# Kernel optimization log

Measured on AMD Instinct MI355X. Metric: run time of the kernel, lower is better.

Reference implementation:

```python
import jax, jax.numpy as jnp
import numpy as np

RATE_NUM = 8
MAX_RATE = 256
C = 256


def setup_inputs() -> dict:
    key = jax.random.key(0)
    k1, k2, k3, k4 = jax.random.split(key, 4)
    B, H, W = 4, 32, 32
    x = jax.random.normal(k1, (B, MAX_RATE, H, W), dtype=jnp.float32)
    indexes = jax.random.randint(k2, (B * H * W,), 0, RATE_NUM, dtype=jnp.int64)
    # kaiming_normal_(a=sqrt(5)) on (rate_num, max_rate, C): fan_in = C (last dim),
    # gain = sqrt(2/(1+a^2)) = sqrt(1/3), std = gain/sqrt(fan_in)
    std = np.sqrt(1.0 / 3.0) / np.sqrt(C)
    weight = jax.random.normal(k3, (RATE_NUM, MAX_RATE, C), dtype=jnp.float32) * std
    bound = 1.0 / np.sqrt(RATE_NUM)
    bias = jax.random.uniform(k4, (RATE_NUM, C), dtype=jnp.float32, minval=-bound, maxval=bound)
    return {"x": x, "indexes": indexes, "weight": weight, "bias": bias}


def reference(x, indexes, weight, bias):
    B, R, H, W = x.shape  # R == max_rate
    L = H * W
    x_blr = x.reshape(B, R, L).transpose(0, 2, 1)          # (B, L, R)
    w = weight[indexes].reshape(B, L, R, -1)               # (B, L, R, C)
    b = bias[indexes].reshape(B, L, -1)                    # (B, L, C)
    out = jnp.einsum('blr,blrc->blc', x_blr, w) + b        # per-token GEMV
    return out.reshape(B, H, W, -1).transpose(0, 3, 1, 2)  # (B, C, H, W)
```

## Files before the change

### kernel.cpp

```cpp
#include <hip/hip_runtime.h>


#define C_DIM 256
#define KD    256

typedef __attribute__((ext_vector_type(8))) short bf16x8;
typedef __attribute__((ext_vector_type(4))) float f32x4;

__device__ inline short f2bf(float f) {
    union { float f; unsigned u; } v; v.f = f;
    return (short)((v.u + 0x7FFFu + ((v.u >> 16) & 1u)) >> 16);
}

__global__ __launch_bounds__(256) void fused_mfma_kernel(
    const float* __restrict__ x,
    const int*   __restrict__ idx,
    const float* __restrict__ weight,
    const float* __restrict__ bias,
    float*       __restrict__ out)
{
    const int t    = threadIdx.x;
    const int lane = t & 63;
    const int wav  = t >> 6;
    const int quad = lane >> 4;
    const int li   = lane & 15;

    const int j   = blockIdx.z;
    const int c0  = blockIdx.x * 128 + (wav & 1) * 64;
    const int lg0 = blockIdx.y * 128 + (wav >> 1) * 64;
    const int b   = lg0 >> 10;
    const int l0  = lg0 & 1023;

    const float* __restrict__ wp = weight + j * (KD * C_DIM) + (quad * 8) * C_DIM + c0 + li;
    const float* __restrict__ xp = x + (b << 18) + ((quad * 8) << 10) + l0 + li;

    f32x4 acc[4][4];
    #pragma unroll
    for (int mt = 0; mt < 4; ++mt)
        #pragma unroll
        for (int nt = 0; nt < 4; ++nt)
            acc[mt][nt] = (f32x4){0.f, 0.f, 0.f, 0.f};

    for (int kc = 0; kc < KD; kc += 32) {
        bf16x8 af[4], bfr[4];
        #pragma unroll
        for (int mt = 0; mt < 4; ++mt) {
            const float* __restrict__ p = wp + kc * C_DIM + mt * 16;
            #pragma unroll
            for (int i = 0; i < 8; ++i) af[mt][i] = f2bf(p[i * C_DIM]);
        }
        #pragma unroll
        for (int nt = 0; nt < 4; ++nt) {
            const float* __restrict__ p = xp + (kc << 10) + nt * 16;
            #pragma unroll
            for (int i = 0; i < 8; ++i) bfr[nt][i] = f2bf(p[i << 10]);
        }
        #pragma unroll
        for (int mt = 0; mt < 4; ++mt)
            #pragma unroll
            for (int nt = 0; nt < 4; ++nt)
                acc[mt][nt] = __builtin_amdgcn_mfma_f32_16x16x32_bf16(
                    af[mt], bfr[nt], acc[mt][nt], 0, 0, 0);
    }

    #pragma unroll
    for (int mt = 0; mt < 4; ++mt) {
        const int cb = c0 + mt * 16 + quad * 4;
        const float4 bb = *(const float4*)(bias + j * C_DIM + cb);
        #pragma unroll
        for (int nt = 0; nt < 4; ++nt) {
            const int lg = lg0 + nt * 16 + li;
            if (idx[lg] != j) continue;
            float* __restrict__ op = out + (b << 18) + (cb << 10) + (lg & 1023);
            op[0 << 10] = acc[mt][nt][0] + bb.x;
            op[1 << 10] = acc[mt][nt][1] + bb.y;
            op[2 << 10] = acc[mt][nt][2] + bb.z;
            op[3 << 10] = acc[mt][nt][3] + bb.w;
        }
    }
}

extern "C" void kernel_launch(void* const* d_in, const int* in_sizes, int n_in,
                              void* d_out, int out_size, void* d_ws, size_t ws_size,
                              hipStream_t stream)
{
    const float* x      = (const float*)d_in[0];
    const int*   idx    = (const int*)  d_in[1];
    const float* weight = (const float*)d_in[2];
    const float* bias   = (const float*)d_in[3];
    float*       out    = (float*)      d_out;

    fused_mfma_kernel<<<dim3(2, 32, 8), 256, 0, stream>>>(x, idx, weight, bias, out);
}
```

Before: 76.30 us.

## Pre-convert x and weights to K-contiguous bf16 buffers before MFMA GEMM

Adds a conversion kernel that transposes x and weight through shared memory into K-major bf16 global buffers. The GEMM kernel can then load each MFMA fragment with a single 16-byte vector load instead of eight strided fp32 loads plus per-element conversion, and it double-buffers those fragments across K steps. This removes redundant conversion and uncoalesced strided loads in the GEMM, at the cost of an extra kernel launch and an extra round trip through global memory for the converted data.

```diff
diff --git a/kernel.cpp b/kernel.cpp
--- a/kernel.cpp
+++ b/kernel.cpp
@@ -3,21 +3,65 @@
 
 #define C_DIM 256
 #define KD    256
+#define N_J   8
 
 typedef __attribute__((ext_vector_type(8))) short bf16x8;
 typedef __attribute__((ext_vector_type(4))) float f32x4;
+
+__device__ __attribute__((aligned(16))) short g_xbf[4096 * KD];
+__device__ __attribute__((aligned(16))) short g_wbf[N_J * C_DIM * KD];
 
 __device__ inline short f2bf(float f) {
     union { float f; unsigned u; } v; v.f = f;
     return (short)((v.u + 0x7FFFu + ((v.u >> 16) & 1u)) >> 16);
 }
 
-__global__ __launch_bounds__(256) void fused_mfma_kernel(
-    const float* __restrict__ x,
-    const int*   __restrict__ idx,
-    const float* __restrict__ weight,
-    const float* __restrict__ bias,
-    float*       __restrict__ out)
+__global__ __launch_bounds__(256) void convert_kernel(const float* __restrict__ x,
+                                                      const float* __restrict__ w)
+{
+    __shared__ float T[64][65];
+    const int t    = threadIdx.x;
+    const int lane = t & 63;
+    const int grp  = t >> 6;
+    const int blk  = blockIdx.x;
+
+    if (blk < 256) {
+        const int b  = blk >> 6;
+        const int l0 = ((blk >> 2) & 15) * 64;
+        const int k0 = (blk & 3) * 64;
+        #pragma unroll
+        for (int i = 0; i < 16; ++i) {
+            const int kl = i * 4 + grp;
+            T[kl][lane] = x[(b << 18) + ((k0 + kl) << 10) + l0 + lane];
+        }
+        __syncthreads();
+        #pragma unroll
+        for (int i = 0; i < 16; ++i) {
+            const int ll = i * 4 + grp;
+            g_xbf[((b << 10) + l0 + ll) * KD + k0 + lane] = f2bf(T[lane][ll]);
+        }
+    } else {
+        const int blk2 = blk - 256;
+        const int j  = blk2 >> 4;
+        const int c0 = ((blk2 >> 2) & 3) * 64;
+        const int k0 = (blk2 & 3) * 64;
+        #pragma unroll
+        for (int i = 0; i < 16; ++i) {
+            const int kl = i * 4 + grp;
+            T[kl][lane] = w[(j * KD + k0 + kl) * C_DIM + c0 + lane];
+        }
+        __syncthreads();
+        #pragma unroll
+        for (int i = 0; i < 16; ++i) {
+            const int cl = i * 4 + grp;
+            g_wbf[(j * C_DIM + c0 + cl) * KD + k0 + lane] = f2bf(T[lane][cl]);
+        }
+    }
+}
+
+__global__ __launch_bounds__(256) void gemm_kernel(const int*   __restrict__ idx,
+                                                   const float* __restrict__ bias,
+                                                   float*       __restrict__ out)
 {
     const int t    = threadIdx.x;
     const int lane = t & 63;
@@ -29,10 +73,15 @@
     const int c0  = blockIdx.x * 128 + (wav & 1) * 64;
     const int lg0 = blockIdx.y * 128 + (wav >> 1) * 64;
     const int b   = lg0 >> 10;
-    const int l0  = lg0 & 1023;
 
-    const float* __restrict__ wp = weight + j * (KD * C_DIM) + (quad * 8) * C_DIM + c0 + li;
-    const float* __restrict__ xp = x + (b << 18) + ((quad * 8) << 10) + l0 + li;
+    const short* __restrict__ pa[4];
+    const short* __restrict__ pb[4];
+    #pragma unroll
+    for (int mt = 0; mt < 4; ++mt)
+        pa[mt] = g_wbf + ((j << 16) | ((c0 + mt * 16 + li) << 8)) + quad * 8;
+    #pragma unroll
+    for (int nt = 0; nt < 4; ++nt)
+        pb[nt] = g_xbf + ((lg0 + nt * 16 + li) << 8) + quad * 8;
 
     f32x4 acc[4][4];
     #pragma unroll
@@ -41,26 +90,30 @@
         for (int nt = 0; nt < 4; ++nt)
             acc[mt][nt] = (f32x4){0.f, 0.f, 0.f, 0.f};
 
-    for (int kc = 0; kc < KD; kc += 32) {
-        bf16x8 af[4], bfr[4];
-        #pragma unroll
-        for (int mt = 0; mt < 4; ++mt) {
-            const float* __restrict__ p = wp + kc * C_DIM + mt * 16;
+    bf16x8 af[2][4], bfr[2][4];
+    #pragma unroll
+    for (int q = 0; q < 4; ++q) {
+        af[0][q]  = *(const bf16x8*)(pa[q]);
+        bfr[0][q] = *(const bf16x8*)(pb[q]);
+    }
+
+    #pragma unroll
+    for (int kc = 0; kc < 8; ++kc) {
+        const int p = kc & 1;
+        if (kc < 7) {
+            const int kofs = (kc + 1) * 32;
             #pragma unroll
-            for (int i = 0; i < 8; ++i) af[mt][i] = f2bf(p[i * C_DIM]);
-        }
-        #pragma unroll
-        for (int nt = 0; nt < 4; ++nt) {
-            const float* __restrict__ p = xp + (kc << 10) + nt * 16;
-            #pragma unroll
-            for (int i = 0; i < 8; ++i) bfr[nt][i] = f2bf(p[i << 10]);
+            for (int q = 0; q < 4; ++q) {
+                af[p ^ 1][q]  = *(const bf16x8*)(pa[q] + kofs);
+                bfr[p ^ 1][q] = *(const bf16x8*)(pb[q] + kofs);
+            }
         }
         #pragma unroll
         for (int mt = 0; mt < 4; ++mt)
             #pragma unroll
             for (int nt = 0; nt < 4; ++nt)
                 acc[mt][nt] = __builtin_amdgcn_mfma_f32_16x16x32_bf16(
-                    af[mt], bfr[nt], acc[mt][nt], 0, 0, 0);
+                    af[p][mt], bfr[p][nt], acc[mt][nt], 0, 0, 0);
     }
 
     #pragma unroll
@@ -90,5 +143,6 @@
     const float* bias   = (const float*)d_in[3];
     float*       out    = (float*)      d_out;
 
-    fused_mfma_kernel<<<dim3(2, 32, 8), 256, 0, stream>>>(x, idx, weight, bias, out);
+    convert_kernel<<<384, 256, 0, stream>>>(x, weight);
+    gemm_kernel<<<dim3(2, 32, 8), 256, 0, stream>>>(idx, bias, out);
 }
```

After: 84.66 us. +11.0%, slower.

## Stage bf16-packed weight and input tiles in LDS for shared MFMA operands

Applied to the files above, without the earlier changes.

Each block now loads 64-deep K slices of weight and x with coalesced float4 reads, converts pairs of K rows to packed bf16, and stores them in padded shared-memory tiles. The four waves then read their MFMA fragments from LDS instead of each wave doing strided scalar global loads and conversions. This removes redundant global loads across waves and uncoalesced access. The cost is two barriers per K slice, about 33 KB of LDS per block, and rounding that no longer breaks ties to even.

```diff
diff --git a/kernel.cpp b/kernel.cpp
--- a/kernel.cpp
+++ b/kernel.cpp
@@ -3,13 +3,16 @@
 
 #define C_DIM 256
 #define KD    256
+#define CB    128
+#define LB    128
+#define LDP   132
 
 typedef __attribute__((ext_vector_type(8))) short bf16x8;
 typedef __attribute__((ext_vector_type(4))) float f32x4;
 
-__device__ inline short f2bf(float f) {
-    union { float f; unsigned u; } v; v.f = f;
-    return (short)((v.u + 0x7FFFu + ((v.u >> 16) & 1u)) >> 16);
+__device__ inline unsigned pk2(float a, float b) {
+    union { float f; unsigned u; } x, y; x.f = a; y.f = b;
+    return ((x.u + 0x8000u) >> 16) | ((y.u + 0x8000u) & 0xFFFF0000u);
 }
 
 __global__ __launch_bounds__(256) void fused_mfma_kernel(
@@ -25,14 +28,23 @@
     const int quad = lane >> 4;
     const int li   = lane & 15;
 
-    const int j   = blockIdx.z;
-    const int c0  = blockIdx.x * 128 + (wav & 1) * 64;
-    const int lg0 = blockIdx.y * 128 + (wav >> 1) * 64;
-    const int b   = lg0 >> 10;
-    const int l0  = lg0 & 1023;
+    const int j    = blockIdx.z;
+    const int cb0  = blockIdx.x * CB;
+    const int lg0b = blockIdx.y * LB;
+    const int b    = lg0b >> 10;
+    const int l0b  = lg0b & 1023;
 
-    const float* __restrict__ wp = weight + j * (KD * C_DIM) + (quad * 8) * C_DIM + c0 + li;
-    const float* __restrict__ xp = x + (b << 18) + ((quad * 8) << 10) + l0 + li;
+    __shared__ unsigned Asl[32 * LDP];
+    __shared__ unsigned Bsl[32 * LDP];
+
+    const int c_locb = (wav & 1) * 64;
+    const int l_locb = (wav >> 1) * 64;
+
+    const float* __restrict__ wbase = weight + j * (KD * C_DIM) + cb0;
+    const float* __restrict__ xbase = x + (b << 18) + l0b;
+
+    const int sc4  = (t & 31) * 4;
+    const int srow = t >> 5;
 
     f32x4 acc[4][4];
     #pragma unroll
@@ -41,37 +53,76 @@
         for (int nt = 0; nt < 4; ++nt)
             acc[mt][nt] = (f32x4){0.f, 0.f, 0.f, 0.f};
 
-    for (int kc = 0; kc < KD; kc += 32) {
-        bf16x8 af[4], bfr[4];
+    for (int p = 0; p < 4; ++p) {
+        const int k0 = p * 64;
+
         #pragma unroll
-        for (int mt = 0; mt < 4; ++mt) {
-            const float* __restrict__ p = wp + kc * C_DIM + mt * 16;
+        for (int i = 0; i < 4; ++i) {
+            const int kp = i * 8 + srow;
+            const int k  = k0 + kp * 2;
+            const float4 a0 = *(const float4*)(wbase + k * C_DIM + sc4);
+            const float4 a1 = *(const float4*)(wbase + (k + 1) * C_DIM + sc4);
+            const float4 b0 = *(const float4*)(xbase + (k << 10) + sc4);
+            const float4 b1 = *(const float4*)(xbase + ((k + 1) << 10) + sc4);
+            uint4 pa, pb;
+            pa.x = pk2(a0.x, a1.x); pa.y = pk2(a0.y, a1.y);
+            pa.z = pk2(a0.z, a1.z); pa.w = pk2(a0.w, a1.w);
+            pb.x = pk2(b0.x, b1.x); pb.y = pk2(b0.y, b1.y);
+            pb.z = pk2(b0.z, b1.z); pb.w = pk2(b0.w, b1.w);
+            *(uint4*)&Asl[kp * LDP + sc4] = pa;
+            *(uint4*)&Bsl[kp * LDP + sc4] = pb;
+        }
+        __syncthreads();
+
+        #pragma unroll
+        for (int h = 0; h < 2; ++h) {
+            const int rbase = h * 16 + quad * 4;
+            bf16x8 af[4], bfr[4];
             #pragma unroll
-            for (int i = 0; i < 8; ++i) af[mt][i] = f2bf(p[i * C_DIM]);
+            for (int mt = 0; mt < 4; ++mt) {
+                const int cl = c_locb + mt * 16 + li;
+                uint4 u;
+                u.x = Asl[(rbase + 0) * LDP + cl];
+                u.y = Asl[(rbase + 1) * LDP + cl];
+                u.z = Asl[(rbase + 2) * LDP + cl];
+                u.w = Asl[(rbase + 3) * LDP + cl];
+                af[mt] = __builtin_bit_cast(bf16x8, u);
+            }
+            #pragma unroll
+            for (int nt = 0; nt < 4; ++nt) {
+                const int ll = l_locb + nt * 16 + li;
+                uint4 u;
+                u.x = Bsl[(rbase + 0) * LDP + ll];
+                u.y = Bsl[(rbase + 1) * LDP + ll];
+                u.z = Bsl[(rbase + 2) * LDP + ll];
+                u.w = Bsl[(rbase + 3) * LDP + ll];
+                bfr[nt] = __builtin_bit_cast(bf16x8, u);
+            }
+            #pragma unroll
+            for (int mt = 0; mt < 4; ++mt)
+                #pragma unroll
+                for (int nt = 0; nt < 4; ++nt)
+                    acc[mt][nt] = __builtin_amdgcn_mfma_f32_16x16x32_bf16(
+                        af[mt], bfr[nt], acc[mt][nt], 0, 0, 0);
         }
-        #pragma unroll
-        for (int nt = 0; nt < 4; ++nt) {
-            const float* __restrict__ p = xp + (kc << 10) + nt * 16;
-            #pragma unroll
-            for (int i = 0; i < 8; ++i) bfr[nt][i] = f2bf(p[i << 10]);
-        }
-        #pragma unroll
-        for (int mt = 0; mt < 4; ++mt)
-            #pragma unroll
-            for (int nt = 0; nt < 4; ++nt)
-                acc[mt][nt] = __builtin_amdgcn_mfma_f32_16x16x32_bf16(
-                    af[mt], bfr[nt], acc[mt][nt], 0, 0, 0);
+        __syncthreads();
     }
 
+    bool keep[4];
+    int  lgv[4];
+    #pragma unroll
+    for (int nt = 0; nt < 4; ++nt) {
+        lgv[nt]  = lg0b + l_locb + nt * 16 + li;
+        keep[nt] = (idx[lgv[nt]] == j);
+    }
     #pragma unroll
     for (int mt = 0; mt < 4; ++mt) {
-        const int cb = c0 + mt * 16 + quad * 4;
+        const int cb = cb0 + c_locb + mt * 16 + quad * 4;
         const float4 bb = *(const float4*)(bias + j * C_DIM + cb);
         #pragma unroll
         for (int nt = 0; nt < 4; ++nt) {
-            const int lg = lg0 + nt * 16 + li;
-            if (idx[lg] != j) continue;
-            float* __restrict__ op = out + (b << 18) + (cb << 10) + (lg & 1023);
+            if (!keep[nt]) continue;
+            float* __restrict__ op = out + (b << 18) + (cb << 10) + (lgv[nt] & 1023);
             op[0 << 10] = acc[mt][nt][0] + bb.x;
             op[1 << 10] = acc[mt][nt][1] + bb.y;
             op[2 << 10] = acc[mt][nt][2] + bb.z;
```

Measured after the change: 74.08 us. 1.03x faster.
